# Performance work log

Measured on AMD Instinct MI355X. Metric: run time of the kernel, lower is better.

## Reference

```python
import jax, jax.numpy as jnp
import numpy as np
import math

T, P, ITERS, H = 6, 8, 2, 8          # nr_types, num_proto, iters, n_head
D, F = 512, 1024                      # dim_proto, feature_dim (hidden_dim==D)
L = T * ITERS                         # 12 cross-attention layers


def _ln(x, g=None, b=None, eps=1e-5):
    m = x.mean(-1, keepdims=True)
    v = x.var(-1, keepdims=True)
    y = (x - m) * jax.lax.rsqrt(v + eps)
    if g is not None:
        y = y * g + b
    return y


def _forward(x_batch, batch_mask, node_type, pm_W, pm_b, pm_g, pm_bn,
             proto_logsigma, rand_mul, Wq, bq, Wk, bk, Wv, bv, Wo, bo,
             ag, ab, Wm1, bm1, lg, lb, Wm2, bm2, pg, pb):
    B, N, _ = x_batch.shape
    dt = x_batch.dtype
    bm = batch_mask.astype(dt)                                   # [B,N]
    onehot = jax.nn.one_hot(node_type, T, dtype=dt)              # [B,N,T]
    valid = bm * jnp.any(x_batch != 0, axis=-1).astype(dt)       # [B,N]
    mbt = onehot * valid[:, :, None]                             # [B,N,T]
    sums = jnp.einsum('bnt,bnf->btf', mbt, x_batch)              # per-(batch,type) sum
    cnt = mbt.sum(1)                                             # [B,T]
    fallback = x_batch.sum(1) / bm.sum(1, keepdims=True)         # [B,F]
    proto_mu = jnp.where(cnt[..., None] > 0,
                         sums / jnp.maximum(cnt, 1.0)[..., None],
                         fallback[:, None, :])                   # [B,T,F]

    # proto_mlp: Linear + LayerNorm + GELU (dropout = eval/identity)
    mu = jax.nn.gelu(_ln(proto_mu @ pm_W + pm_b, pm_g, pm_bn), approximate=False)  # [B,T,D]
    all_proto = mu[:, :, None, :] + jnp.exp(proto_logsigma)[None] * rand_mul[None]  # [B,T,P,D]

    dh = D // H
    scale = 1.0 / math.sqrt(dh)
    keymask = bm[:, None, None, :] == 0                          # [B,1,1,N]

    def layer(q, i):
        resid = q                                                 # [B,P,D]
        k = _ln((x_batch @ Wk[i] + bk[i]).reshape(B, N, H, dh))   # QK-LayerNorm (no affine)
        v = (x_batch @ Wv[i] + bv[i]).reshape(B, N, H, dh)
        qh = _ln((q @ Wq[i] + bq[i]).reshape(B, P, H, dh))
        dots = jnp.einsum('bkhd,bnhd->bkhn', qh, k) * scale       # [B,P,H,N]
        dots = jnp.where(keymask, -jnp.inf, dots)
        attn = jax.nn.softmax(dots, axis=-1)
        upd = jnp.einsum('bnhd,bkhn->bkhd', v, attn).reshape(B, P, D)
        upd = upd @ Wo[i] + bo[i]
        q = resid + _ln(upd, ag[i], ab[i])
        h = jax.nn.gelu(_ln(q @ Wm1[i] + bm1[i], lg[i], lb[i]), approximate=False)
        h = h @ Wm2[i] + bm2[i]
        return q + _ln(h, pg[i], pb[i])

    outs = []
    c = 0
    for i in range(T):
        p = all_proto[:, i]
        for _ in range(ITERS):
            p = layer(p, c)
            c += 1
        outs.append(p)
    prototypes = jnp.stack(outs, axis=1)                          # [B,T,P,D]
    return prototypes, proto_mu


def setup_inputs() -> dict:
    key = jax.random.key(0)
    ks = jax.random.split(key, 40)
    B, N = 4, 4096
    sc = 0.02

    def rn(i, shape, s=sc):
        return jax.random.normal(ks[i], shape, jnp.float32) * s

    inp = {
        'x_batch': jax.random.normal(ks[0], (B, N, F), jnp.float32),
        'batch_mask': jax.random.randint(ks[1], (B, N), 0, 2, jnp.int32),
        'node_type': jax.random.randint(ks[2], (B, N), 0, T, jnp.int32),
        'pm_W': rn(3, (F, D)), 'pm_b': jnp.zeros((D,)),
        'pm_g': jnp.ones((D,)), 'pm_bn': jnp.zeros((D,)),
        'proto_logsigma': rn(4, (T, 1, D), 0.05),
        'rand_mul': jax.random.normal(ks[5], (T, P, D), jnp.float32),
        'Wq': rn(6, (L, D, D)), 'bq': jnp.zeros((L, D)),
        'Wk': rn(7, (L, F, D)), 'bk': jnp.zeros((L, D)),
        'Wv': rn(8, (L, F, D)), 'bv': jnp.zeros((L, D)),
        'Wo': rn(9, (L, D, D)), 'bo': jnp.zeros((L, D)),
        'ag': jnp.ones((L, D)), 'ab': jnp.zeros((L, D)),
        'Wm1': rn(10, (L, D, D)), 'bm1': jnp.zeros((L, D)),
        'lg': jnp.ones((L, D)), 'lb': jnp.zeros((L, D)),
        'Wm2': rn(11, (L, D, D)), 'bm2': jnp.zeros((L, D)),
        'pg': jnp.ones((L, D)), 'pb': jnp.zeros((L, D)),
    }
    return inp


def reference(x_batch, batch_mask, node_type, pm_W, pm_b, pm_g, pm_bn,
              proto_logsigma, rand_mul, Wq, bq, Wk, bk, Wv, bv, Wo, bo,
              ag, ab, Wm1, bm1, lg, lb, Wm2, bm2, pg, pb):
    return _forward(x_batch, batch_mask, node_type, pm_W, pm_b, pm_g, pm_bn,
                    proto_logsigma, rand_mul, Wq, bq, Wk, bk, Wv, bv, Wo, bo,
                    ag, ab, Wm1, bm1, lg, lb, Wm2, bm2, pg, pb)
```

## Files before the change

### kernel.cpp

```cpp
#include <hip/hip_runtime.h>
#include <hip/hip_bf16.h>
#include <stdint.h>

#define TT 6
#define PP 8
#define HH 8
#define DD 512
#define FF 1024
#define DH 64
#define NB 4
#define NN 4096
#define LL 12
#define NCH 16
#define CHK 256

typedef __attribute__((ext_vector_type(8))) short short8v;
typedef __attribute__((ext_vector_type(4))) float f32x4;
typedef __attribute__((ext_vector_type(4))) unsigned short u16x4;
typedef __attribute__((ext_vector_type(8))) unsigned short u16x8;
typedef unsigned short u16;

__device__ __forceinline__ float bf2f(u16 u){
  union { unsigned int i; float f; } x; x.i = ((unsigned int)u) << 16; return x.f;
}
// ... 6 lines not shown
  #pragma unroll
  for (int o = 32; o > 0; o >>= 1) x += __shfl_xor(x, o);
  return x;
}
__device__ __forceinline__ float ldf(const void* p, size_t i, int f32){
  float v;
  if (f32) v = ((const float*)p)[i];
  else     v = bf2f(((const u16*)p)[i]);
  return v;
}
__device__ __forceinline__ float gemv_vec(const float* __restrict__ xs,
    const void* __restrict__ W, size_t wbase, int ktot, int wf32,
    float* __restrict__ red, int tid){
  int g = tid & 63, sl = tid >> 6;
  int kpw = ktot >> 3;
  float a[8] = {0,0,0,0,0,0,0,0};
  if (wf32){
    const float* Wp = (const float*)W + wbase + (size_t)(sl*kpw)*DD + g*8;
    #pragma unroll 4
    for (int i = 0; i < kpw; ++i){
      float xv = xs[sl*kpw + i];
      f32x4 lo = *(const f32x4*)(Wp + (size_t)i*DD);
      f32x4 hi = *(const f32x4*)(Wp + (size_t)i*DD + 4);
      a[0]+=xv*lo.x; a[1]+=xv*lo.y; a[2]+=xv*lo.z; a[3]+=xv*lo.w;
      a[4]+=xv*hi.x; a[5]+=xv*hi.y; a[6]+=xv*hi.z; a[7]+=xv*hi.w;
    }
  } else {
    const u16* Wp = (const u16*)W + wbase + (size_t)(sl*kpw)*DD + g*8;
    #pragma unroll 4
    for (int i = 0; i < kpw; ++i){
      float xv = xs[sl*kpw + i];
      u16x8 w8 = *(const u16x8*)(Wp + (size_t)i*DD);
      #pragma unroll
      for (int j = 0; j < 8; ++j) a[j] += xv * bf2f(w8[j]);
    }
  }
  #pragma unroll
  for (int j = 0; j < 8; ++j) red[sl*512 + g*8 + j] = a[j];
  __syncthreads();
  float y = 0;
  #pragma unroll
  for (int s2 = 0; s2 < 8; ++s2) y += red[s2*512 + tid];
  return y;
}
__device__ __forceinline__ void glds16(const void* g, void* l){
#if __has_builtin(__builtin_amdgcn_global_load_lds)
  __builtin_amdgcn_global_load_lds(
      (const __attribute__((address_space(1))) void*)g,
      (__attribute__((address_space(3))) void*)l, 16, 0, 0);
#else
  *(u16x8*)l = *(const u16x8*)g;
#endif
}
__device__ __forceinline__ void tail_gemm(f32x4 acc[2][4], const u16* __restrict__ Bp,
    const u16* As, int l15, int q4, int n0w){
  #pragma unroll
  for (int mi = 0; mi < 2; ++mi)
    #pragma unroll
    for (int ni = 0; ni < 4; ++ni){ f32x4 z = {0,0,0,0}; acc[mi][ni] = z; }
  #pragma unroll 2
  for (int k0 = 0; k0 < 512; k0 += 32){
    short8v bf[4], af[2];
    #pragma unroll
    for (int ni = 0; ni < 4; ++ni)
      bf[ni] = *(const short8v*)(Bp + (size_t)(n0w + ni*16 + l15)*DD + k0 + q4*8);
    #pragma unroll
    for (int mi = 0; mi < 2; ++mi)
      af[mi] = *(const short8v*)(As + (mi*16 + l15)*520 + k0 + q4*8);
    #pragma unroll
    for (int mi = 0; mi < 2; ++mi)
      #pragma unroll
      for (int ni = 0; ni < 4; ++ni)
        acc[mi][ni] = __builtin_amdgcn_mfma_f32_16x16x32_bf16(af[mi], bf[ni], acc[mi][ni], 0, 0, 0);
  }
}
__device__ __forceinline__ void row_ln(const f32x4 acc[2][4],
    float* red1, float* red2, int w, int l15, int q4,
    float mv[2][4], float rv[2][4]){
  float s1[2][4], s2[2][4];
  #pragma unroll
  for (int mi = 0; mi < 2; ++mi)
    #pragma unroll
    for (int r = 0; r < 4; ++r){
      float a0=acc[mi][0][r], a1=acc[mi][1][r], a2=acc[mi][2][r], a3=acc[mi][3][r];
      s1[mi][r] = (a0+a1)+(a2+a3);
      s2[mi][r] = (a0*a0+a1*a1)+(a2*a2+a3*a3);
    }
  #pragma unroll
  for (int o = 1; o < 16; o <<= 1)
    #pragma unroll
    for (int mi = 0; mi < 2; ++mi)
      #pragma unroll
      for (int r = 0; r < 4; ++r){
        s1[mi][r] += __shfl_xor(s1[mi][r], o);
        s2[mi][r] += __shfl_xor(s2[mi][r], o);
      }
  if (l15 == 0){
    #pragma unroll
    for (int mi = 0; mi < 2; ++mi)
      #pragma unroll
      for (int r = 0; r < 4; ++r){
        int row = mi*16 + q4*4 + r;
        red1[row*8 + w] = s1[mi][r];
        red2[row*8 + w] = s2[mi][r];
      }
  }
  __syncthreads();
  #pragma unroll
  for (int mi = 0; mi < 2; ++mi)
    #pragma unroll
    for (int r = 0; r < 4; ++r){
      int row = mi*16 + q4*4 + r;
      float S1 = 0, S2 = 0;
      #pragma unroll
      for (int j = 0; j < 8; ++j){ S1 += red1[row*8+j]; S2 += red2[row*8+j]; }
      float m = S1 * (1.f/DD);
      float var = S2 * (1.f/DD) - m*m;
      mv[mi][r] = m;
      rv[mi][r] = rsqrtf(var + 1e-5f);
    }
  __syncthreads();
}

__global__ void k_detect(const void* __restrict__ X, int* __restrict__ flag){
  int tid = threadIdx.x;
  const u16* u = (const u16*)X;
  int bad = 0;
  for (int i = tid; i < 8192; i += 256){
    int ex = (u[i] >> 7) & 0xFF;
    if (ex >= 0x90) bad = 1;
  }
  __shared__ int s;
  if (tid == 0) s = 0;
  __syncthreads();
  if (bad) s = 1;
  __syncthreads();
  if (tid == 0) *flag = s;
}

__global__ void k_xbv(const void* __restrict__ X, u16* __restrict__ Xb,
                      const int* __restrict__ bm, float* __restrict__ valid,
                      const int* __restrict__ flagp){
  int f32 = *flagp;
  int bid = blockIdx.x, tid = threadIdx.x;
  size_t idx = (size_t)bid*FF + tid*4;
  bool a;
  if (f32){
    f32x4 v = *(const f32x4*)((const float*)X + idx);
    u16x4 o; o.x=f2bf(v.x); o.y=f2bf(v.y); o.z=f2bf(v.z); o.w=f2bf(v.w);
    *(u16x4*)(Xb+idx) = o;
    a = (v.x!=0.f)||(v.y!=0.f)||(v.z!=0.f)||(v.w!=0.f);
  } else {
    u16x4 v = *(const u16x4*)((const u16*)X + idx);
    *(u16x4*)(Xb+idx) = v;
    a = (bf2f(v.x)!=0.f)||(bf2f(v.y)!=0.f)||(bf2f(v.z)!=0.f)||(bf2f(v.w)!=0.f);
  }
  __shared__ int flag;
  if (tid==0) flag = 0;
  __syncthreads();
  if (a) flag = 1;
  __syncthreads();
  if (tid==0) valid[bid] = (flag && bm[bid]) ? 1.f : 0.f;
}

__global__ void k_compact(const int* __restrict__ bm, int* __restrict__ nidx,
                          int* __restrict__ cntc){
  int b = blockIdx.x, tid = threadIdx.x;
  __shared__ int csum[256];
  __shared__ int pref[257];
  int base = b*NN + tid*16;
  int f[16]; int loc = 0;
  #pragma unroll
  for (int i = 0; i < 16; ++i){ f[i] = (bm[base+i] != 0); loc += f[i]; }
// ... 119 lines not shown
  int bt = blockIdx.x; int b = bt/TT, t = bt%TT;
  int d = threadIdx.x;
  __shared__ float xs[FF];
  __shared__ float red[4096];
  __shared__ float r1[8], r2[8];
  xs[d] = proto_mu[(size_t)bt*FF + d];
  xs[d+512] = proto_mu[(size_t)bt*FF + d + 512];
  __syncthreads();
  float acc = ldf(pmb, d, f32) + gemv_vec(xs, pmW, 0, FF, f32, red, d);
  int lane = d & 63, wid = d >> 6;
  float s1 = wave_sum(acc), s2 = wave_sum(acc*acc);
  if (lane==0){ r1[wid]=s1; r2[wid]=s2; }
  __syncthreads();
  float m=0, qq=0;
  #pragma unroll
  for (int i=0;i<8;++i){ m+=r1[i]; qq+=r2[i]; }
  m *= (1.f/DD); float var = qq*(1.f/DD) - m*m;
  float y = (acc - m) * rsqrtf(var + 1e-5f) * ldf(pmg, d, f32) + ldf(pmbn, d, f32);
  float mu = 0.5f * y * (1.f + erff(y * 0.70710678118654752f));
  #pragma unroll
  for (int p = 0; p < PP; ++p){
    float rv = ldf(rmul, (size_t)(t*PP+p)*DD + d, f32);
    float ls = ldf(lsig, (size_t)t*DD + d, f32);
    qstate[(((size_t)(b*TT+t))*PP + p)*DD + d] = mu + expf(ls) * rv;
  }
}

__global__ void k_transpose(const void* __restrict__ Wk, const void* __restrict__ Wv,
                            u16* __restrict__ TK, u16* __restrict__ TV,
                            int tlo, int s, const int* __restrict__ flagp){
  int f32 = *flagp;
  int ti = blockIdx.z >> 1, kv = blockIdx.z & 1;
  int c = 2*(tlo+ti)+s;
  size_t eoff = (size_t)c*FF*DD;
  const void* W = kv ? Wv : Wk;
  u16* T = (kv ? TV : TK) + (size_t)ti*FF*DD;
  __shared__ u16 tile[32][33];
  int n0 = blockIdx.x * 32, k0 = blockIdx.y * 32;
  int tx = threadIdx.x, ty = threadIdx.y;
  #pragma unroll
  for (int i = 0; i < 4; ++i){
    size_t idx = eoff + (size_t)(k0 + ty + i*8)*DD + n0 + tx;
    u16 v;
    if (f32) v = f2bf(((const float*)W)[idx]);
    else     v = ((const u16*)W)[idx];
    tile[ty + i*8][tx] = v;
  }
  __syncthreads();
  #pragma unroll
  for (int i = 0; i < 4; ++i)
    T[(size_t)(n0 + ty + i*8)*FF + k0 + tx] = tile[tx][ty + i*8];
}

__global__ void __launch_bounds__(512) k_kvgemm(const u16* __restrict__ Xb,
    const u16* __restrict__ TK, const u16* __restrict__ TV,
    const void* __restrict__ bk, const void* __restrict__ bv,
    u16* __restrict__ Kb, u16* __restrict__ Vb,
    const int* __restrict__ nidx, const int* __restrict__ cntc,
    int tlo, int s, int nt, const int* __restrict__ flagp){
  int f32 = *flagp;
  int orig = blockIdx.x;
  int x = orig & 7, r = orig >> 3;
  int bx = r / nt, pr = r - bx*nt;
  int pairg = x*nt + pr;
  int by = pairg & 3; int kvti = pairg >> 2; int kv = kvti & 1; int ti = kvti >> 1;
  int b = bx >> 4, jt = bx & 15;
  int cnt = cntc[b];
  if (jt*256 >= cnt) return;
  int c = 2*(tlo+ti)+s;
  size_t boff = (size_t)c*DD;
  const u16* WT = (kv ? TV : TK) + (size_t)ti*FF*DD;
  const void* bias = kv ? bv : bk;
  u16* out = (kv ? Vb : Kb) + (size_t)ti*((size_t)NB*NN*DD);
  int n0 = by*128;
  __shared__ __align__(16) char LDS[3*24576];
  int tid = threadIdx.x, wid = tid >> 6, lane = tid & 63;
  int wr = wid >> 1, wcn = wid & 1;
  const u16* gp0; const u16* gp1; const u16* gp2;
  int lo0, lo1, lo2;
  {
    const u16* gps[3]; int los[3];
    #pragma unroll
    for (int i = 0; i < 3; ++i){
      int e = tid + i*512;
      if (e < 1024){
        int row = e>>2, sp = e&3;
        int ssrc = sp ^ (((row>>3)&1)<<1);
        int cl = jt*256 + row; if (cl >= cnt) cl = cnt-1;
        int grow = nidx[b*NN + cl];
        gps[i] = Xb + ((size_t)b*NN + grow)*FF + ssrc*8;
        los[i] = e*16;
      } else {
        int e2 = e - 1024;
        int row = e2>>2, sp = e2&3;
        int ssrc = sp ^ (((row>>3)&1)<<1);
        gps[i] = WT + (size_t)(n0 + row)*FF + ssrc*8;
        los[i] = 16384 + e2*16;
      }
    }
    gp0=gps[0]; gp1=gps[1]; gp2=gps[2];
    lo0=los[0]; lo1=los[1]; lo2=los[2];
  }
#define STAGE(T) { char* bb_ = LDS + ((T)%3)*24576; \
  glds16(gp0 + (T)*32, bb_ + lo0); glds16(gp1 + (T)*32, bb_ + lo1); \
  glds16(gp2 + (T)*32, bb_ + lo2); }
  int ke = (lane>>4) ^ (((lane>>3)&1)<<1);
  int arow[4], brow[4];
  #pragma unroll
  for (int mi = 0; mi < 4; ++mi)
    arow[mi] = (wr*64 + mi*16 + (lane&15))*64 + ke*16;
  #pragma unroll
  for (int ni = 0; ni < 4; ++ni)
    brow[ni] = 16384 + (wcn*64 + ni*16 + (lane&15))*64 + ke*16;
  f32x4 acc[4][4] = {};
  STAGE(0);
  STAGE(1);
  asm volatile("s_waitcnt vmcnt(3)" ::: "memory");
  __builtin_amdgcn_sched_barrier(0);
  __builtin_amdgcn_s_barrier();
  __builtin_amdgcn_sched_barrier(0);
  #pragma unroll
  for (int t = 0; t < 32; ++t){
    const char* Bbuf = LDS + (t%3)*24576;
    short8v af[4], bf[4];
    #pragma unroll
    for (int mi = 0; mi < 4; ++mi)
      af[mi] = *(const short8v*)(Bbuf + arow[mi]);
    #pragma unroll
    for (int ni = 0; ni < 4; ++ni)
      bf[ni] = *(const short8v*)(Bbuf + brow[ni]);
    if (t + 2 <= 31) STAGE(t+2);
    __builtin_amdgcn_s_setprio(1);
    #pragma unroll
    for (int mi = 0; mi < 4; ++mi)
      #pragma unroll
      for (int ni = 0; ni < 4; ++ni)
        acc[mi][ni] = __builtin_amdgcn_mfma_f32_16x16x32_bf16(af[mi], bf[ni], acc[mi][ni], 0, 0, 0);
    __builtin_amdgcn_s_setprio(0);
    if (t < 30)       asm volatile("s_waitcnt vmcnt(3)" ::: "memory");
    else if (t == 30) asm volatile("s_waitcnt vmcnt(0)" ::: "memory");
    __builtin_amdgcn_sched_barrier(0);
    if (t < 31){
      __builtin_amdgcn_s_barrier();
      __builtin_amdgcn_sched_barrier(0);
    }
  }
#undef STAGE
  #pragma unroll
  for (int mi = 0; mi < 4; ++mi){
    #pragma unroll
    for (int ni = 0; ni < 4; ++ni){
      int col = n0 + wcn*64 + ni*16 + (lane & 15);
      float bvf = ldf(bias, boff + col, f32);
      #pragma unroll
      for (int r2 = 0; r2 < 4; ++r2){
        int row = jt*256 + wr*64 + mi*16 + (lane>>4)*4 + r2;
        out[((size_t)b*NN + row)*DD + col] = f2bf(acc[mi][ni][r2] + bvf);
      }
    }
  }
}

__global__ void __launch_bounds__(512) k_qproj(const float* __restrict__ qstate,
      const void* __restrict__ Wq, const void* __restrict__ bq,
      float* __restrict__ qh, int tlo, int s, int wmode,
      const int* __restrict__ flagp){
  int f32 = *flagp;
  int wf32 = wmode ? f32 : 0;
  int z = blockIdx.x; int ti = z >> 5, rr = z & 31;
  int b = rr >> 3, p = rr & 7;
  int t = tlo + ti, c = 2*t + s;
  size_t woff = (size_t)c*DD*DD, boff = (size_t)c*DD;
  int d = threadIdx.x;
  __shared__ float xs[DD];
  __shared__ float red[4096];
  const float* xrow = qstate + (((size_t)(b*TT+t))*PP + p)*DD;
  xs[d] = xrow[d];
  __syncthreads();
  float acc = ldf(bq, boff + d, f32) + gemv_vec(xs, Wq, woff, DD, wf32, red, d);
  float s1 = wave_sum(acc) * (1.f/DH);
  float s2 = wave_sum(acc*acc) * (1.f/DH);
  float var = s2 - s1*s1;
  qh[(size_t)z*DD + d] = (acc - s1) * rsqrtf(var + 1e-5f);
}

__global__ void __launch_bounds__(512) k_attnA(const u16* __restrict__ Kb,
     const u16* __restrict__ Vb, const float* __restrict__ qh,
     const int* __restrict__ cntc, float* __restrict__ Opart, float* __restrict__ lpart){
  int ic = blockIdx.x, bh = blockIdx.y, ti = blockIdx.z;
  int b = bh >> 3, h = bh & 7;
  int cnt = cntc[b];
  if (ic*CHK >= cnt) return;
  int tid = threadIdx.x, p8 = tid >> 6, ln = tid & 63;
  int r8 = ln >> 3, g = ln & 7;
  __shared__ __align__(16) char KV[65536];
  __shared__ float qs[PP*DH];
  __shared__ float qsum[PP];
  __shared__ float e_lds[CHK*9];
  int rem = cnt - ic*CHK;
  float qv = qh[((size_t)(ti*32 + b*PP + p8))*DD + h*DH + ln];
  size_t tioff = (size_t)ti*((size_t)NB*NN*DD);
  const u16* Kbase = Kb + tioff + ((size_t)(b*NN) + (size_t)ic*CHK)*DD + h*DH;
  const u16* Vbase = Vb + tioff + ((size_t)(b*NN) + (size_t)ic*CHK)*DD + h*DH;
  #pragma unroll
  for (int i = 0; i < 4; ++i){
    int e = tid + i*512;
    int row = e >> 3, sp = e & 7;
    int rr = row < rem ? row : rem-1;
    glds16(Kbase + (size_t)rr*DD + sp*8, (char*)KV + e*16);
// ... 47 lines not shown
    }
    float dg = (g==0)?ap[0]:(g==1)?ap[1]:(g==2)?ap[2]:(g==3)?ap[3]
             : (g==4)?ap[4]:(g==5)?ap[5]:(g==6)?ap[6]:ap[7];
    float sv = (dg - sm*qsum[g]) * inv * 0.125f;
    e_lds[nl*9 + g] = (nl < rem) ? __expf(sv) : 0.f;
  }
  __syncthreads();
  {
    float lp = 0;
    #pragma unroll
    for (int j = 0; j < CHK/64; ++j) lp += e_lds[(ln + j*64)*9 + p8];
    lp = wave_sum(lp);
    if (ln == 0) lpart[((size_t)(ti*32+bh)*NCH + ic)*PP + p8] = lp;
  }
  {
    float a0=0,a1=0,a2=0,a3=0,a4=0,a5=0,a6=0,a7=0;
    int vseg = (r8 ^ g) * 16;
    #pragma unroll 4
    for (int m = 0; m < CHK/8; ++m){
      float e = e_lds[(g + m*8)*9 + p8];
      u16x8 vv = *(const u16x8*)((const char*)KV + 32768 + (g + m*8)*128 + vseg);
      a0 += e*bf2f(vv[0]); a1 += e*bf2f(vv[1]);
      a2 += e*bf2f(vv[2]); a3 += e*bf2f(vv[3]);
      a4 += e*bf2f(vv[4]); a5 += e*bf2f(vv[5]);
      a6 += e*bf2f(vv[6]); a7 += e*bf2f(vv[7]);
    }
    #pragma unroll
    for (int o = 1; o < 8; o <<= 1){
      a0 += __shfl_xor(a0, o); a1 += __shfl_xor(a1, o);
      a2 += __shfl_xor(a2, o); a3 += __shfl_xor(a3, o);
      a4 += __shfl_xor(a4, o); a5 += __shfl_xor(a5, o);
      a6 += __shfl_xor(a6, o); a7 += __shfl_xor(a7, o);
    }
    if (g == 0){
      float* op = Opart + ((size_t)(ti*32+bh)*NCH + ic)*512 + p8*64 + r8*8;
      f32x4 lo = {a0,a1,a2,a3}, hi = {a4,a5,a6,a7};
      *(f32x4*)op = lo;
      *((f32x4*)op + 1) = hi;
    }
  }
}

__global__ void __launch_bounds__(512) k_tailm(
    const float* __restrict__ Opart, const float* __restrict__ lpart,
    const int* __restrict__ cntc,
    float* __restrict__ qstate, float* __restrict__ qh,
    const u16* __restrict__ Wt,
    const void* __restrict__ bo, const void* __restrict__ ag, const void* __restrict__ ab,
    const void* __restrict__ bm1, const void* __restrict__ lg, const void* __restrict__ lb,
    const void* __restrict__ bm2, const void* __restrict__ pg, const void* __restrict__ pb,
    const void* __restrict__ bq,
    int tlo, int s, const int* __restrict__ flagp){
  int f32 = *flagp;
  int ti = blockIdx.x;
  int t = tlo + ti, c = 2*t + s;
  int tid = threadIdx.x;
  int w = tid >> 6, lane = tid & 63, q4 = lane >> 4, l15 = lane & 15;
  int n0w = w*64;
  size_t boff = (size_t)c*DD;
  const size_t famSz = (size_t)LL*DD*DD;
  __shared__ u16 As[32*520];
  __shared__ float red1[256], red2[256];
  __shared__ float lval[256];
  if (tid < 256){
    int row = tid >> 3, hh = tid & 7;
    int b = row >> 3, p = row & 7;
    int nch = (cntc[b] + CHK - 1) / CHK;
    float l = 0;
    for (int ic = 0; ic < nch; ++ic)
      l += lpart[((size_t)(ti*32 + b*8 + hh)*NCH + ic)*PP + p];
    lval[tid] = 1.f / l;
  }
  __syncthreads();
  {
    int hh = tid >> 6, dd = tid & 63;
    for (int row = 0; row < 32; ++row){
      int b = row >> 3, p = row & 7;
      int nch = (cntc[b] + CHK - 1) / CHK;
      float o = 0;
      for (int ic = 0; ic < nch; ++ic)
        o += Opart[((size_t)(ti*32 + b*8 + hh)*NCH + ic)*512 + p*64 + dd];
      As[row*520 + tid] = f2bf(o * lval[row*8 + hh]);
    }
  }
  __syncthreads();
  f32x4 acc[2][4], q2[2][4];
  float mv[2][4], rv[2][4];
  {
    const u16* Bp = Wt + famSz + (size_t)c*DD*DD;
    tail_gemm(acc, Bp, As, l15, q4, n0w);
    #pragma unroll
    for (int ni = 0; ni < 4; ++ni){
      float bv = ldf(bo, boff + n0w + ni*16 + l15, f32);
      #pragma unroll
      for (int mi = 0; mi < 2; ++mi)
        #pragma unroll
        for (int r = 0; r < 4; ++r) acc[mi][ni][r] += bv;
    }
    row_ln(acc, red1, red2, w, l15, q4, mv, rv);
    #pragma unroll
    for (int ni = 0; ni < 4; ++ni){
      int col = n0w + ni*16 + l15;
      float gm = ldf(ag, boff + col, f32), bt = ldf(ab, boff + col, f32);
      #pragma unroll
      for (int mi = 0; mi < 2; ++mi)
        #pragma unroll
        for (int r = 0; r < 4; ++r){
          int row = mi*16 + q4*4 + r;
          int b = row >> 3, p = row & 7;
          size_t qoff = (((size_t)(b*TT+t))*PP + p)*DD;
          float y = (acc[mi][ni][r] - mv[mi][r])*rv[mi][r]*gm + bt;
          q2[mi][ni][r] = qstate[qoff + col] + y;
        }
    }
    #pragma unroll
    for (int mi = 0; mi < 2; ++mi)
      #pragma unroll
      for (int r = 0; r < 4; ++r){
        int row = mi*16 + q4*4 + r;
        #pragma unroll
        for (int ni = 0; ni < 4; ++ni)
          As[row*520 + n0w + ni*16 + l15] = f2bf(q2[mi][ni][r]);
      }
  }
  __syncthreads();
  {
    const u16* Bp = Wt + 2*famSz + (size_t)c*DD*DD;
    tail_gemm(acc, Bp, As + 0, l15, q4, n0w);
    #pragma unroll
    for (int ni = 0; ni < 4; ++ni){
      float bv = ldf(bm1, boff + n0w + ni*16 + l15, f32);
      #pragma unroll
      for (int mi = 0; mi < 2; ++mi)
        #pragma unroll
        for (int r = 0; r < 4; ++r) acc[mi][ni][r] += bv;
    }
    row_ln(acc, red1, red2, w, l15, q4, mv, rv);
    #pragma unroll
    for (int ni = 0; ni < 4; ++ni){
      int col = n0w + ni*16 + l15;
      float gm = ldf(lg, boff + col, f32), bt = ldf(lb, boff + col, f32);
      #pragma unroll
      for (int mi = 0; mi < 2; ++mi)
        #pragma unroll
        for (int r = 0; r < 4; ++r){
          int row = mi*16 + q4*4 + r;
          float y = (acc[mi][ni][r] - mv[mi][r])*rv[mi][r]*gm + bt;
          y = 0.5f*y*(1.f + erff(y*0.70710678118654752f));
          As[row*520 + col] = f2bf(y);
        }
    }
  }
  __syncthreads();
  {
    const u16* Bp = Wt + 3*famSz + (size_t)c*DD*DD;
    tail_gemm(acc, Bp, As, l15, q4, n0w);
    #pragma unroll
    for (int ni = 0; ni < 4; ++ni){
      float bv = ldf(bm2, boff + n0w + ni*16 + l15, f32);
      #pragma unroll
      for (int mi = 0; mi < 2; ++mi)
        #pragma unroll
        for (int r = 0; r < 4; ++r) acc[mi][ni][r] += bv;
    }
    row_ln(acc, red1, red2, w, l15, q4, mv, rv);
    #pragma unroll
    for (int ni = 0; ni < 4; ++ni){
      int col = n0w + ni*16 + l15;
      float gm = ldf(pg, boff + col, f32), bt = ldf(pb, boff + col, f32);
      #pragma unroll
      for (int mi = 0; mi < 2; ++mi)
        #pragma unroll
        for (int r = 0; r < 4; ++r){
          int row = mi*16 + q4*4 + r;
          int b = row >> 3, p = row & 7;
          size_t qoff = (((size_t)(b*TT+t))*PP + p)*DD;
          float outv = q2[mi][ni][r] + (acc[mi][ni][r] - mv[mi][r])*rv[mi][r]*gm + bt;
          qstate[qoff + col] = outv;
          if (s == 0) As[row*520 + col] = f2bf(outv);
        }
    }
  }
  if (s == 0){
    __syncthreads();
    const u16* Bp = Wt + (size_t)(c+1)*DD*DD;
    tail_gemm(acc, Bp, As, l15, q4, n0w);
    #pragma unroll
    for (int ni = 0; ni < 4; ++ni){
      float bv = ldf(bq, (size_t)(c+1)*DD + n0w + ni*16 + l15, f32);
      #pragma unroll
      for (int mi = 0; mi < 2; ++mi)
        #pragma unroll
        for (int r = 0; r < 4; ++r) acc[mi][ni][r] += bv;
    }
    float s1[2][4], s2[2][4];
    #pragma unroll
    for (int mi = 0; mi < 2; ++mi)
      #pragma unroll
      for (int r = 0; r < 4; ++r){
        float a0=acc[mi][0][r], a1=acc[mi][1][r], a2=acc[mi][2][r], a3=acc[mi][3][r];
        s1[mi][r] = (a0+a1)+(a2+a3);
        s2[mi][r] = (a0*a0+a1*a1)+(a2*a2+a3*a3);
      }
    #pragma unroll
    for (int o = 1; o < 16; o <<= 1)
      #pragma unroll
      for (int mi = 0; mi < 2; ++mi)
        #pragma unroll
        for (int r = 0; r < 4; ++r){
          s1[mi][r] += __shfl_xor(s1[mi][r], o);
          s2[mi][r] += __shfl_xor(s2[mi][r], o);
        }
    #pragma unroll
    for (int mi = 0; mi < 2; ++mi)
      #pragma unroll
      for (int r = 0; r < 4; ++r){
        int row = mi*16 + q4*4 + r;
        float m = s1[mi][r] * (1.f/DH);
        float var = s2[mi][r] * (1.f/DH) - m*m;
        float ri = rsqrtf(var + 1e-5f);
        #pragma unroll
        for (int ni = 0; ni < 4; ++ni){
          int col = n0w + ni*16 + l15;
          qh[((size_t)(ti*32 + row))*DD + col] = (acc[mi][ni][r] - m)*ri;
        }
      }
  }
}

__global__ void __launch_bounds__(512) k_tail(
    const float* __restrict__ Opart, const float* __restrict__ lpart,
    const int* __restrict__ cntc,
    float* __restrict__ qstate, float* __restrict__ qh,
    const void* __restrict__ Wo_, const void* __restrict__ Wm1_,
    const void* __restrict__ Wm2_, const void* __restrict__ Wq_,
    const void* __restrict__ bo, const void* __restrict__ ag, const void* __restrict__ ab,
    const void* __restrict__ bm1, const void* __restrict__ lg, const void* __restrict__ lb,
    const void* __restrict__ bm2, const void* __restrict__ pg, const void* __restrict__ pb,
    const void* __restrict__ bq,
    int tlo, int s, int wmode, const int* __restrict__ flagp){
  int f32 = *flagp;
  int wf32 = wmode ? f32 : 0;
  int z = blockIdx.x; int ti = z >> 5, rr = z & 31;
  int b = rr >> 3, p = rr & 7;
  int t = tlo + ti, c = 2*t + s;
  int d = threadIdx.x;
  int h = d >> 6, dd = d & 63;
  int lane = d & 63, wid = d >> 6;
  size_t qoff = (((size_t)(b*TT+t))*PP + p)*DD;
  size_t boff = (size_t)c*DD;
  size_t w0 = (size_t)c*DD*DD;
  __shared__ float xs[DD];
  __shared__ float red[4096];
  __shared__ float r1[8], r2[8];
  int nch = (cntc[b] + CHK - 1) / CHK;
  float o = 0, l = 0;
  for (int ic = 0; ic < nch; ++ic){
    o += Opart[((size_t)(ti*32 + b*8 + h)*NCH + ic)*512 + p*64 + dd];
    l += lpart[((size_t)(ti*32 + b*8 + h)*NCH + ic)*PP + p];
  }
  float upd = o / l;
  xs[d] = upd;
  __syncthreads();
  float acc = ldf(bo, boff + d, f32) + gemv_vec(xs, Wo_, w0, DD, wf32, red, d);
  {
    float s1 = wave_sum(acc), s2 = wave_sum(acc*acc);
    if (lane == 0){ r1[wid] = s1; r2[wid] = s2; }
  }
  __syncthreads();
  float m = 0, qv = 0;
  #pragma unroll
  for (int i = 0; i < 8; ++i){ m += r1[i]; qv += r2[i]; }
  m *= (1.f/DD); float var = qv*(1.f/DD) - m*m;
  float y = (acc - m)*rsqrtf(var + 1e-5f)*ldf(ag, boff+d, f32) + ldf(ab, boff+d, f32);
  float q2 = qstate[qoff + d] + y;
  __syncthreads();
  xs[d] = q2;
  __syncthreads();
  float acc2 = ldf(bm1, boff + d, f32) + gemv_vec(xs, Wm1_, w0, DD, wf32, red, d);
// ... 71 lines not shown
  float* bmsum    = (float*)(ws + 512);
  float* colsums  = (float*)(ws + 768);
  float* coltotal = (float*)(ws + 99072);
  float* valid    = (float*)(ws + 115456);
  float* proto_mu = (float*)(ws + 180992);
  float* qstate   = (float*)(ws + 279296);
  int*   cntc     = (int*)(ws + 672512);
  int*   nidx     = (int*)(ws + 672768);

  size_t off = 738304;
  auto take = [&](size_t bytes)->char*{
    char* p = ws + off; off = (off + bytes + 255) & ~(size_t)255; return p;
  };
  u16* Xbf = (u16*)take((size_t)NB*NN*FF*2);

  const size_t perT = (size_t)65536
                    + 16384
                    + 1048576
                    + 2*1048576
                    + 2*16777216;
  size_t base = off;
  int nt = 1;
  if      (ws_size >= base + 6*perT + 65536) nt = 6;
  else if (ws_size >= base + 3*perT + 65536) nt = 3;
  else if (ws_size >= base + 2*perT + 65536) nt = 2;

  float* qh    = (float*)take((size_t)nt*65536);
  float* lpart = (float*)take((size_t)nt*16384);
  float* Opart = (float*)take((size_t)nt*1048576);
  u16*   WkT   = (u16*)take((size_t)nt*1048576);
  u16*   WvT   = (u16*)take((size_t)nt*1048576);
  u16*   Kb    = (u16*)take((size_t)nt*16777216);
  u16*   Vb    = (u16*)take((size_t)nt*16777216);

  const size_t wtBytes = (size_t)4*LL*DD*DD*2;
  int useWt = (ws_size >= off + wtBytes + 65536) ? 1 : 0;
  u16* Wt = useWt ? (u16*)take(wtBytes) : nullptr;

  hipMemsetAsync(ws + 256, 0, 115200, stream);
  k_detect<<<1, 256, 0, stream>>>(X, flagp);
  k_xbv<<<NB*NN, 256, 0, stream>>>(X, Xbf, bm, valid, flagp);
  k_compact<<<NB, 256, 0, stream>>>(bm, nidx, cntc);
  if (useWt)
    k_wbfT<<<dim3(16, 16, 4*LL), dim3(32, 8), 0, stream>>>(Wq, Wo, Wm1, Wm2, Wt, flagp);
  k_cnt<<<NB, 256, 0, stream>>>(valid, bm, ntype, cnt, bmsum);
  k_colsum<<<dim3(1, 64, NB), 256, 0, stream>>>(Xbf, valid, ntype, colsums, coltotal);
  k_protomu<<<NB*TT, 256, 0, stream>>>(colsums, coltotal, cnt, bmsum, proto_mu, d_out, flagp);
  k_mu<<<NB*TT, 512, 0, stream>>>(proto_mu, pmW, pmb, pmg, pmbn, lsig, rmul, qstate, flagp);

  for (int tlo = 0; tlo < TT; tlo += nt){
    for (int s = 0; s < 2; ++s){
      k_transpose<<<dim3(16, 32, 2*nt), dim3(32, 8), 0, stream>>>(
          Wk, Wv, WkT, WvT, tlo, s, flagp);
      k_kvgemm<<<64*8*nt, 512, 0, stream>>>(
          Xbf, WkT, WvT, bk, bv, Kb, Vb, nidx, cntc, tlo, s, nt, flagp);
      if (s == 0)
        k_qproj<<<nt*32, 512, 0, stream>>>(qstate, Wq, bq, qh, tlo, s, 1, flagp);
      k_attnA<<<dim3(NCH, 32, nt), 512, 0, stream>>>(Kb, Vb, qh, cntc, Opart, lpart);
      if (useWt)
        k_tailm<<<nt, 512, 0, stream>>>(Opart, lpart, cntc, qstate, qh, Wt,
            bo, ag, ab, bm1, lg, lb, bm2, pg, pb, bq, tlo, s, flagp);
      else
        k_tail<<<nt*32, 512, 0, stream>>>(Opart, lpart, cntc, qstate, qh,
            Wo, Wm1, Wm2, Wq, bo, ag, ab, bm1, lg, lb, bm2, pg, pb, bq,
            tlo, s, 1, flagp);
    }
  }
  k_out<<<NB*TT*PP*DD/256, 256, 0, stream>>>(qstate, d_out, flagp);
}
```

Measured before the change: 693.7 us.

## Enlarge K/V GEMM tile to 256x256 with 4-stage split A/B LDS pipeline

The K/V projection GEMM now uses 256x256 output tiles per workgroup instead of 256x128, so each block does twice the work and the grid is halved. Each wave now accumulates a 128x64 sub-tile. A and B are staged into separate 4-deep LDS ring buffers, and loads are interleaved between half-tile MFMA groups. Block indexing is remapped so blocks are grouped per XCD. The aim is more data reuse per LDS byte and fewer redundant X loads. In exchange, register pressure rises (32 accumulators) and 128KB of LDS limits occupancy, with more barriers per k-step.

```diff
diff --git a/kernel.cpp b/kernel.cpp
--- a/kernel.cpp
+++ b/kernel.cpp
@@ -374,7 +374,21 @@
     T[(size_t)(n0 + ty + i*8)*FF + k0 + tx] = tile[tx][ty + i*8];
 }
 
-__global__ void __launch_bounds__(512) k_kvgemm(const u16* __restrict__ Xb,
+#define PBAR() { __builtin_amdgcn_sched_barrier(0); \
+                 __builtin_amdgcn_s_barrier(); \
+                 __builtin_amdgcn_sched_barrier(0); }
+
+template<int MH>
+__device__ __forceinline__ void mfma_q(f32x4 (&acc)[8][4],
+    const short8v (&af)[4], const short8v (&bf)[4]){
+  #pragma unroll
+  for (int i = 0; i < 4; ++i)
+    #pragma unroll
+    for (int j = 0; j < 4; ++j)
+      acc[MH*4+i][j] = __builtin_amdgcn_mfma_f32_16x16x32_bf16(af[i], bf[j], acc[MH*4+i][j], 0, 0, 0);
+}
+
+__global__ void __launch_bounds__(512, 2) k_kvgemm(const u16* __restrict__ Xb,
     const u16* __restrict__ TK, const u16* __restrict__ TV,
     const void* __restrict__ bk, const void* __restrict__ bv,
     u16* __restrict__ Kb, u16* __restrict__ Vb,
@@ -382,11 +396,13 @@
     int tlo, int s, int nt, const int* __restrict__ flagp){
   int f32 = *flagp;
   int orig = blockIdx.x;
-  int x = orig & 7, r = orig >> 3;
-  int bx = r / nt, pr = r - bx*nt;
-  int pairg = x*nt + pr;
-  int by = pairg & 3; int kvti = pairg >> 2; int kv = kvti & 1; int ti = kvti >> 1;
-  int b = bx >> 4, jt = bx & 15;
+  int nwg = gridDim.x;
+  int cpx = nwg >> 3;
+  int wgid = (orig & 7)*cpx + (orig >> 3);
+  int grp = 4*nt;
+  int aid = wgid / grp, inner = wgid - aid*grp;
+  int b = aid >> 4, jt = aid & 15;
+  int by = inner & 1, kv = (inner >> 1) & 1, ti = inner >> 2;
   int cnt = cntc[b];
   if (jt*256 >= cnt) return;
   int c = 2*(tlo+ti)+s;
@@ -394,89 +410,89 @@
   const u16* WT = (kv ? TV : TK) + (size_t)ti*FF*DD;
   const void* bias = kv ? bv : bk;
   u16* out = (kv ? Vb : Kb) + (size_t)ti*((size_t)NB*NN*DD);
-  int n0 = by*128;
-  __shared__ __align__(16) char LDS[3*24576];
+  int n0 = by*256;
+  __shared__ __align__(16) char LDS[131072];
   int tid = threadIdx.x, wid = tid >> 6, lane = tid & 63;
-  int wr = wid >> 1, wcn = wid & 1;
-  const u16* gp0; const u16* gp1; const u16* gp2;
-  int lo0, lo1, lo2;
-  {
-    const u16* gps[3]; int los[3];
-    #pragma unroll
-    for (int i = 0; i < 3; ++i){
-      int e = tid + i*512;
-      if (e < 1024){
-        int row = e>>2, sp = e&3;
-        int ssrc = sp ^ (((row>>3)&1)<<1);
-        int cl = jt*256 + row; if (cl >= cnt) cl = cnt-1;
-        int grow = nidx[b*NN + cl];
-        gps[i] = Xb + ((size_t)b*NN + grow)*FF + ssrc*8;
-        los[i] = e*16;
-      } else {
-        int e2 = e - 1024;
-        int row = e2>>2, sp = e2&3;
-        int ssrc = sp ^ (((row>>3)&1)<<1);
-        gps[i] = WT + (size_t)(n0 + row)*FF + ssrc*8;
-        los[i] = 16384 + e2*16;
-      }
-    }
-    gp0=gps[0]; gp1=gps[1]; gp2=gps[2];
-    lo0=los[0]; lo1=los[1]; lo2=los[2];
-  }
-#define STAGE(T) { char* bb_ = LDS + ((T)%3)*24576; \
-  glds16(gp0 + (T)*32, bb_ + lo0); glds16(gp1 + (T)*32, bb_ + lo1); \
-  glds16(gp2 + (T)*32, bb_ + lo2); }
-  int ke = (lane>>4) ^ (((lane>>3)&1)<<1);
-  int arow[4], brow[4];
-  #pragma unroll
-  for (int mi = 0; mi < 4; ++mi)
-    arow[mi] = (wr*64 + mi*16 + (lane&15))*64 + ke*16;
-  #pragma unroll
-  for (int ni = 0; ni < 4; ++ni)
-    brow[ni] = 16384 + (wcn*64 + ni*16 + (lane&15))*64 + ke*16;
-  f32x4 acc[4][4] = {};
-  STAGE(0);
-  STAGE(1);
-  asm volatile("s_waitcnt vmcnt(3)" ::: "memory");
-  __builtin_amdgcn_sched_barrier(0);
-  __builtin_amdgcn_s_barrier();
-  __builtin_amdgcn_sched_barrier(0);
-  #pragma unroll
-  for (int t = 0; t < 32; ++t){
-    const char* Bbuf = LDS + (t%3)*24576;
+  int wr = wid >> 2, wc = wid & 3;
+  int l15 = lane & 15;
+  int keo = ((lane>>4) ^ (((lane>>3)&1)<<1)) * 16;
+  int abase = (wr*128 + l15)*64 + keo;
+  int bbase = (wc*64  + l15)*64 + keo;
+  int row0 = tid >> 2, sp = tid & 3;
+  int ssrc = sp ^ (((row0>>3)&1)<<1);
+  int cl0 = jt*256 + row0;        if (cl0 >= cnt) cl0 = cnt-1;
+  int cl1 = jt*256 + row0 + 128;  if (cl1 >= cnt) cl1 = cnt-1;
+  const u16* pA0 = Xb + ((size_t)b*NN + nidx[b*NN+cl0])*FF + ssrc*8;
+  const u16* pA1 = Xb + ((size_t)b*NN + nidx[b*NN+cl1])*FF + ssrc*8;
+  const u16* pB0 = WT + (size_t)(n0 + row0)*FF + ssrc*8;
+  const u16* pB1 = WT + (size_t)(n0 + row0 + 128)*FF + ssrc*8;
+  int la0 = tid*16, la1 = la0 + 8192;
+#define STA(S_) { char* d_ = LDS + ((S_)&3)*16384; \
+  glds16(pA0 + (S_)*32, d_ + la0); glds16(pA1 + (S_)*32, d_ + la1); }
+#define STB(S_) { char* d_ = LDS + 65536 + ((S_)&3)*16384; \
+  glds16(pB0 + (S_)*32, d_ + la0); glds16(pB1 + (S_)*32, d_ + la1); }
+  f32x4 acc[8][4] = {};
+  STA(0); STB(0); STA(1); STB(1); STA(2); STB(2); STA(3);
+  asm volatile("s_waitcnt vmcnt(6)" ::: "memory");
+  PBAR();
+  #pragma unroll 1
+  for (int tk = 0; tk < 16; ++tk){
+    int s0 = 2*tk, s1 = s0 + 1;
+    const char* A0p = LDS + (((tk&1)<<1))*16384;
+    const char* B0p = A0p + 65536;
+    const char* A1p = A0p + 16384;
+    const char* B1p = B0p + 16384;
     short8v af[4], bf[4];
     #pragma unroll
-    for (int mi = 0; mi < 4; ++mi)
-      af[mi] = *(const short8v*)(Bbuf + arow[mi]);
-    #pragma unroll
-    for (int ni = 0; ni < 4; ++ni)
-      bf[ni] = *(const short8v*)(Bbuf + brow[ni]);
-    if (t + 2 <= 31) STAGE(t+2);
+    for (int i = 0; i < 4; ++i) af[i] = *(const short8v*)(A0p + abase + i*1024);
+    #pragma unroll
+    for (int j = 0; j < 4; ++j) bf[j] = *(const short8v*)(B0p + bbase + j*1024);
+    if (tk <= 14) STB(s0+3);
+    PBAR();
     __builtin_amdgcn_s_setprio(1);
-    #pragma unroll
-    for (int mi = 0; mi < 4; ++mi)
-      #pragma unroll
-      for (int ni = 0; ni < 4; ++ni)
-        acc[mi][ni] = __builtin_amdgcn_mfma_f32_16x16x32_bf16(af[mi], bf[ni], acc[mi][ni], 0, 0, 0);
+    mfma_q<0>(acc, af, bf);
     __builtin_amdgcn_s_setprio(0);
-    if (t < 30)       asm volatile("s_waitcnt vmcnt(3)" ::: "memory");
-    else if (t == 30) asm volatile("s_waitcnt vmcnt(0)" ::: "memory");
-    __builtin_amdgcn_sched_barrier(0);
-    if (t < 31){
-      __builtin_amdgcn_s_barrier();
-      __builtin_amdgcn_sched_barrier(0);
-    }
-  }
-#undef STAGE
-  #pragma unroll
-  for (int mi = 0; mi < 4; ++mi){
+    PBAR();
+    #pragma unroll
+    for (int i = 0; i < 4; ++i) af[i] = *(const short8v*)(A0p + abase + 4096 + i*1024);
+    if (tk <= 13) STA(s0+4);
+    PBAR();
+    __builtin_amdgcn_s_setprio(1);
+    mfma_q<1>(acc, af, bf);
+    __builtin_amdgcn_s_setprio(0);
+    PBAR();
+    #pragma unroll
+    for (int i = 0; i < 4; ++i) af[i] = *(const short8v*)(A1p + abase + i*1024);
+    #pragma unroll
+    for (int j = 0; j < 4; ++j) bf[j] = *(const short8v*)(B1p + bbase + j*1024);
+    if (tk <= 13) STB(s1+3);
+    PBAR();
+    __builtin_amdgcn_s_setprio(1);
+    mfma_q<0>(acc, af, bf);
+    __builtin_amdgcn_s_setprio(0);
+    PBAR();
+    #pragma unroll
+    for (int i = 0; i < 4; ++i) af[i] = *(const short8v*)(A1p + abase + 4096 + i*1024);
+    if (tk <= 13) STA(s1+4);
+    if (tk < 14)       { asm volatile("s_waitcnt vmcnt(6)" ::: "memory"); }
+    else if (tk == 14) { asm volatile("s_waitcnt vmcnt(0)" ::: "memory"); }
+    PBAR();
+    __builtin_amdgcn_s_setprio(1);
+    mfma_q<1>(acc, af, bf);
+    __builtin_amdgcn_s_setprio(0);
+    PBAR();
+  }
+#undef STA
+#undef STB
+  #pragma unroll
+  for (int mi = 0; mi < 8; ++mi){
     #pragma unroll
     for (int ni = 0; ni < 4; ++ni){
-      int col = n0 + wcn*64 + ni*16 + (lane & 15);
+      int col = n0 + wc*64 + ni*16 + l15;
       float bvf = ldf(bias, boff + col, f32);
       #pragma unroll
       for (int r2 = 0; r2 < 4; ++r2){
-        int row = jt*256 + wr*64 + mi*16 + (lane>>4)*4 + r2;
+        int row = jt*256 + wr*128 + mi*16 + (lane>>4)*4 + r2;
         out[((size_t)b*NN + row)*DD + col] = f2bf(acc[mi][ni][r2] + bvf);
       }
     }
@@ -980,7 +996,7 @@
     for (int s = 0; s < 2; ++s){
       k_transpose<<<dim3(16, 32, 2*nt), dim3(32, 8), 0, stream>>>(
           Wk, Wv, WkT, WvT, tlo, s, flagp);
-      k_kvgemm<<<64*8*nt, 512, 0, stream>>>(
+      k_kvgemm<<<256*nt, 512, 0, stream>>>(
           Xbf, WkT, WvT, bk, bv, Kb, Vb, nidx, cntc, tlo, s, nt, flagp);
       if (s == 0)
         k_qproj<<<nt*32, 512, 0, stream>>>(qstate, Wq, bq, qh, tlo, s, 1, flagp);
```

Measured after the change: 859.5 us. 23.9% more time.

## Split tail MLP kernel per batch to quadruple block-level parallelism

Applied to the files above, without the earlier changes.

The fused tail kernel (Wo, MLP, next-layer Q projection) previously ran one block per type and handled all 32 query rows. It now launches one block per (type, batch), each handling 8 rows padded to a 16-row MFMA tile. This gives four times as many blocks for the small, latency-bound tail. The cost is that every block streams the full weight matrices, so weight reads rise fourfold, and half of each MFMA tile is wasted on zero padding.

```diff
diff --git a/kernel.cpp b/kernel.cpp
--- a/kernel.cpp
+++ b/kernel.cpp
@@ -82,73 +82,59 @@
   *(u16x8*)l = *(const u16x8*)g;
 #endif
 }
-__device__ __forceinline__ void tail_gemm(f32x4 acc[2][4], const u16* __restrict__ Bp,
+__device__ __forceinline__ void tail_gemm8(f32x4 acc[4], const u16* __restrict__ Bp,
     const u16* As, int l15, int q4, int n0w){
   #pragma unroll
-  for (int mi = 0; mi < 2; ++mi)
-    #pragma unroll
-    for (int ni = 0; ni < 4; ++ni){ f32x4 z = {0,0,0,0}; acc[mi][ni] = z; }
+  for (int ni = 0; ni < 4; ++ni){ f32x4 z = {0,0,0,0}; acc[ni] = z; }
   #pragma unroll 2
   for (int k0 = 0; k0 < 512; k0 += 32){
-    short8v bf[4], af[2];
+    short8v bf[4], af;
     #pragma unroll
     for (int ni = 0; ni < 4; ++ni)
       bf[ni] = *(const short8v*)(Bp + (size_t)(n0w + ni*16 + l15)*DD + k0 + q4*8);
-    #pragma unroll
-    for (int mi = 0; mi < 2; ++mi)
-      af[mi] = *(const short8v*)(As + (mi*16 + l15)*520 + k0 + q4*8);
-    #pragma unroll
-    for (int mi = 0; mi < 2; ++mi)
-      #pragma unroll
-      for (int ni = 0; ni < 4; ++ni)
-        acc[mi][ni] = __builtin_amdgcn_mfma_f32_16x16x32_bf16(af[mi], bf[ni], acc[mi][ni], 0, 0, 0);
-  }
-}
-__device__ __forceinline__ void row_ln(const f32x4 acc[2][4],
+    af = *(const short8v*)(As + l15*520 + k0 + q4*8);
+    #pragma unroll
+    for (int ni = 0; ni < 4; ++ni)
+      acc[ni] = __builtin_amdgcn_mfma_f32_16x16x32_bf16(af, bf[ni], acc[ni], 0, 0, 0);
+  }
+}
+__device__ __forceinline__ void row_ln8(const f32x4 acc[4],
     float* red1, float* red2, int w, int l15, int q4,
-    float mv[2][4], float rv[2][4]){
-  float s1[2][4], s2[2][4];
-  #pragma unroll
-  for (int mi = 0; mi < 2; ++mi)
+    float mv[4], float rv[4]){
+  float s1[4], s2[4];
+  #pragma unroll
+  for (int r = 0; r < 4; ++r){
+    float a0=acc[0][r], a1=acc[1][r], a2=acc[2][r], a3=acc[3][r];
+    s1[r] = (a0+a1)+(a2+a3);
+    s2[r] = (a0*a0+a1*a1)+(a2*a2+a3*a3);
+  }
+  #pragma unroll
+  for (int o = 1; o < 16; o <<= 1)
     #pragma unroll
     for (int r = 0; r < 4; ++r){
-      float a0=acc[mi][0][r], a1=acc[mi][1][r], a2=acc[mi][2][r], a3=acc[mi][3][r];
-      s1[mi][r] = (a0+a1)+(a2+a3);
-      s2[mi][r] = (a0*a0+a1*a1)+(a2*a2+a3*a3);
-    }
-  #pragma unroll
-  for (int o = 1; o < 16; o <<= 1)
-    #pragma unroll
-    for (int mi = 0; mi < 2; ++mi)
-      #pragma unroll
-      for (int r = 0; r < 4; ++r){
-        s1[mi][r] += __shfl_xor(s1[mi][r], o);
-        s2[mi][r] += __shfl_xor(s2[mi][r], o);
-      }
+      s1[r] += __shfl_xor(s1[r], o);
+      s2[r] += __shfl_xor(s2[r], o);
+    }
   if (l15 == 0){
     #pragma unroll
-    for (int mi = 0; mi < 2; ++mi)
-      #pragma unroll
-      for (int r = 0; r < 4; ++r){
-        int row = mi*16 + q4*4 + r;
-        red1[row*8 + w] = s1[mi][r];
-        red2[row*8 + w] = s2[mi][r];
-      }
-  }
-  __syncthreads();
-  #pragma unroll
-  for (int mi = 0; mi < 2; ++mi)
-    #pragma unroll
     for (int r = 0; r < 4; ++r){
-      int row = mi*16 + q4*4 + r;
-      float S1 = 0, S2 = 0;
-      #pragma unroll
-      for (int j = 0; j < 8; ++j){ S1 += red1[row*8+j]; S2 += red2[row*8+j]; }
-      float m = S1 * (1.f/DD);
-      float var = S2 * (1.f/DD) - m*m;
-      mv[mi][r] = m;
-      rv[mi][r] = rsqrtf(var + 1e-5f);
-    }
+      int row = q4*4 + r;
+      red1[row*8 + w] = s1[r];
+      red2[row*8 + w] = s2[r];
+    }
+  }
+  __syncthreads();
+  #pragma unroll
+  for (int r = 0; r < 4; ++r){
+    int row = q4*4 + r;
+    float S1 = 0, S2 = 0;
+    #pragma unroll
+    for (int j = 0; j < 8; ++j){ S1 += red1[row*8+j]; S2 += red2[row*8+j]; }
+    float m = S1 * (1.f/DD);
+    float var = S2 * (1.f/DD) - m*m;
+    mv[r] = m;
+    rv[r] = rsqrtf(var + 1e-5f);
+  }
   __syncthreads();
 }
 
@@ -630,20 +616,21 @@
     const void* __restrict__ bq,
     int tlo, int s, const int* __restrict__ flagp){
   int f32 = *flagp;
-  int ti = blockIdx.x;
+  int z = blockIdx.x;
+  int ti = z >> 2, b = z & 3;
   int t = tlo + ti, c = 2*t + s;
   int tid = threadIdx.x;
   int w = tid >> 6, lane = tid & 63, q4 = lane >> 4, l15 = lane & 15;
   int n0w = w*64;
   size_t boff = (size_t)c*DD;
   const size_t famSz = (size_t)LL*DD*DD;
-  __shared__ u16 As[32*520];
-  __shared__ float red1[256], red2[256];
-  __shared__ float lval[256];
-  if (tid < 256){
-    int row = tid >> 3, hh = tid & 7;
-    int b = row >> 3, p = row & 7;
-    int nch = (cntc[b] + CHK - 1) / CHK;
+  __shared__ u16 As[16*520];
+  __shared__ float red1[128], red2[128];
+  __shared__ float lval[64];
+  int nch = (cntc[b] + CHK - 1) / CHK;
+  for (int i = tid; i < 16*520; i += 512) As[i] = 0;
+  if (tid < 64){
+    int p = tid >> 3, hh = tid & 7;
     float l = 0;
     for (int ic = 0; ic < nch; ++ic)
       l += lpart[((size_t)(ti*32 + b*8 + hh)*NCH + ic)*PP + p];
@@ -652,157 +639,138 @@
   __syncthreads();
   {
     int hh = tid >> 6, dd = tid & 63;
-    for (int row = 0; row < 32; ++row){
-      int b = row >> 3, p = row & 7;
-      int nch = (cntc[b] + CHK - 1) / CHK;
+    #pragma unroll
+    for (int p = 0; p < 8; ++p){
       float o = 0;
       for (int ic = 0; ic < nch; ++ic)
         o += Opart[((size_t)(ti*32 + b*8 + hh)*NCH + ic)*512 + p*64 + dd];
-      As[row*520 + tid] = f2bf(o * lval[row*8 + hh]);
-    }
-  }
-  __syncthreads();
-  f32x4 acc[2][4], q2[2][4];
-  float mv[2][4], rv[2][4];
+      As[p*520 + hh*64 + dd] = f2bf(o * lval[p*8 + hh]);
+    }
+  }
+  __syncthreads();
+  f32x4 acc[4], q2[4];
+  float mv[4], rv[4];
+  size_t qoffb = ((size_t)(b*TT+t))*PP*DD;
   {
     const u16* Bp = Wt + famSz + (size_t)c*DD*DD;
-    tail_gemm(acc, Bp, As, l15, q4, n0w);
+    tail_gemm8(acc, Bp, As, l15, q4, n0w);
     #pragma unroll
     for (int ni = 0; ni < 4; ++ni){
       float bv = ldf(bo, boff + n0w + ni*16 + l15, f32);
       #pragma unroll
-      for (int mi = 0; mi < 2; ++mi)
-        #pragma unroll
-        for (int r = 0; r < 4; ++r) acc[mi][ni][r] += bv;
-    }
-    row_ln(acc, red1, red2, w, l15, q4, mv, rv);
+      for (int r = 0; r < 4; ++r) acc[ni][r] += bv;
+    }
+    row_ln8(acc, red1, red2, w, l15, q4, mv, rv);
     #pragma unroll
     for (int ni = 0; ni < 4; ++ni){
       int col = n0w + ni*16 + l15;
       float gm = ldf(ag, boff + col, f32), bt = ldf(ab, boff + col, f32);
       #pragma unroll
-      for (int mi = 0; mi < 2; ++mi)
-        #pragma unroll
-        for (int r = 0; r < 4; ++r){
-          int row = mi*16 + q4*4 + r;
-          int b = row >> 3, p = row & 7;
-          size_t qoff = (((size_t)(b*TT+t))*PP + p)*DD;
-          float y = (acc[mi][ni][r] - mv[mi][r])*rv[mi][r]*gm + bt;
-          q2[mi][ni][r] = qstate[qoff + col] + y;
-        }
-    }
-    #pragma unroll
-    for (int mi = 0; mi < 2; ++mi)
-      #pragma unroll
       for (int r = 0; r < 4; ++r){
-        int row = mi*16 + q4*4 + r;
+        int row = q4*4 + r;
+        float y = (acc[ni][r] - mv[r])*rv[r]*gm + bt;
+        float res = (q4 < 2) ? qstate[qoffb + (size_t)row*DD + col] : 0.f;
+        q2[ni][r] = res + y;
+      }
+    }
+    if (q4 < 2){
+      #pragma unroll
+      for (int r = 0; r < 4; ++r){
+        int row = q4*4 + r;
         #pragma unroll
         for (int ni = 0; ni < 4; ++ni)
-          As[row*520 + n0w + ni*16 + l15] = f2bf(q2[mi][ni][r]);
+          As[row*520 + n0w + ni*16 + l15] = f2bf(q2[ni][r]);
       }
+    }
   }
   __syncthreads();
   {
     const u16* Bp = Wt + 2*famSz + (size_t)c*DD*DD;
-    tail_gemm(acc, Bp, As + 0, l15, q4, n0w);
+    tail_gemm8(acc, Bp, As, l15, q4, n0w);
     #pragma unroll
     for (int ni = 0; ni < 4; ++ni){
       float bv = ldf(bm1, boff + n0w + ni*16 + l15, f32);
       #pragma unroll
-      for (int mi = 0; mi < 2; ++mi)
-        #pragma unroll
-        for (int r = 0; r < 4; ++r) acc[mi][ni][r] += bv;
-    }
-    row_ln(acc, red1, red2, w, l15, q4, mv, rv);
+      for (int r = 0; r < 4; ++r) acc[ni][r] += bv;
+    }
+    row_ln8(acc, red1, red2, w, l15, q4, mv, rv);
     #pragma unroll
     for (int ni = 0; ni < 4; ++ni){
       int col = n0w + ni*16 + l15;
       float gm = ldf(lg, boff + col, f32), bt = ldf(lb, boff + col, f32);
       #pragma unroll
-      for (int mi = 0; mi < 2; ++mi)
-        #pragma unroll
-        for (int r = 0; r < 4; ++r){
-          int row = mi*16 + q4*4 + r;
-          float y = (acc[mi][ni][r] - mv[mi][r])*rv[mi][r]*gm + bt;
-          y = 0.5f*y*(1.f + erff(y*0.70710678118654752f));
-          As[row*520 + col] = f2bf(y);
-        }
+      for (int r = 0; r < 4; ++r){
+        int row = q4*4 + r;
+        float y = (acc[ni][r] - mv[r])*rv[r]*gm + bt;
+        y = 0.5f*y*(1.f + erff(y*0.70710678118654752f));
+        if (q4 < 2) As[row*520 + col] = f2bf(y);
+      }
     }
   }
   __syncthreads();
   {
     const u16* Bp = Wt + 3*famSz + (size_t)c*DD*DD;
-    tail_gemm(acc, Bp, As, l15, q4, n0w);
+    tail_gemm8(acc, Bp, As, l15, q4, n0w);
     #pragma unroll
     for (int ni = 0; ni < 4; ++ni){
       float bv = ldf(bm2, boff + n0w + ni*16 + l15, f32);
       #pragma unroll
-      for (int mi = 0; mi < 2; ++mi)
-        #pragma unroll
-        for (int r = 0; r < 4; ++r) acc[mi][ni][r] += bv;
-    }
-    row_ln(acc, red1, red2, w, l15, q4, mv, rv);
+      for (int r = 0; r < 4; ++r) acc[ni][r] += bv;
+    }
+    row_ln8(acc, red1, red2, w, l15, q4, mv, rv);
     #pragma unroll
     for (int ni = 0; ni < 4; ++ni){
       int col = n0w + ni*16 + l15;
       float gm = ldf(pg, boff + col, f32), bt = ldf(pb, boff + col, f32);
       #pragma unroll
-      for (int mi = 0; mi < 2; ++mi)
-        #pragma unroll
-        for (int r = 0; r < 4; ++r){
-          int row = mi*16 + q4*4 + r;
-          int b = row >> 3, p = row & 7;
-          size_t qoff = (((size_t)(b*TT+t))*PP + p)*DD;
-          float outv = q2[mi][ni][r] + (acc[mi][ni][r] - mv[mi][r])*rv[mi][r]*gm + bt;
-          qstate[qoff + col] = outv;
+      for (int r = 0; r < 4; ++r){
+        int row = q4*4 + r;
+        float outv = q2[ni][r] + (acc[ni][r] - mv[r])*rv[r]*gm + bt;
+        if (q4 < 2){
+          qstate[qoffb + (size_t)row*DD + col] = outv;
           if (s == 0) As[row*520 + col] = f2bf(outv);
         }
+      }
     }
   }
   if (s == 0){
     __syncthreads();
     const u16* Bp = Wt + (size_t)(c+1)*DD*DD;
-    tail_gemm(acc, Bp, As, l15, q4, n0w);
+    tail_gemm8(acc, Bp, As, l15, q4, n0w);
     #pragma unroll
     for (int ni = 0; ni < 4; ++ni){
       float bv = ldf(bq, (size_t)(c+1)*DD + n0w + ni*16 + l15, f32);
       #pragma unroll
-      for (int mi = 0; mi < 2; ++mi)
-        #pragma unroll
-        for (int r = 0; r < 4; ++r) acc[mi][ni][r] += bv;
-    }
-    float s1[2][4], s2[2][4];
-    #pragma unroll
-    for (int mi = 0; mi < 2; ++mi)
+      for (int r = 0; r < 4; ++r) acc[ni][r] += bv;
+    }
+    float s1[4], s2[4];
+    #pragma unroll
+    for (int r = 0; r < 4; ++r){
+      float a0=acc[0][r], a1=acc[1][r], a2=acc[2][r], a3=acc[3][r];
+      s1[r] = (a0+a1)+(a2+a3);
+      s2[r] = (a0*a0+a1*a1)+(a2*a2+a3*a3);
+    }
+    #pragma unroll
+    for (int o = 1; o < 16; o <<= 1)
       #pragma unroll
       for (int r = 0; r < 4; ++r){
-        float a0=acc[mi][0][r], a1=acc[mi][1][r], a2=acc[mi][2][r], a3=acc[mi][3][r];
-        s1[mi][r] = (a0+a1)+(a2+a3);
-        s2[mi][r] = (a0*a0+a1*a1)+(a2*a2+a3*a3);
+        s1[r] += __shfl_xor(s1[r], o);
+        s2[r] += __shfl_xor(s2[r], o);
       }
-    #pragma unroll
-    for (int o = 1; o < 16; o <<= 1)
-      #pragma unroll
-      for (int mi = 0; mi < 2; ++mi)
-        #pragma unroll
-        for (int r = 0; r < 4; ++r){
-          s1[mi][r] += __shfl_xor(s1[mi][r], o);
-          s2[mi][r] += __shfl_xor(s2[mi][r], o);
-        }
-    #pragma unroll
-    for (int mi = 0; mi < 2; ++mi)
+    if (q4 < 2){
       #pragma unroll
       for (int r = 0; r < 4; ++r){
-        int row = mi*16 + q4*4 + r;
-        float m = s1[mi][r] * (1.f/DH);
-        float var = s2[mi][r] * (1.f/DH) - m*m;
+        int row = q4*4 + r;
+        float m = s1[r] * (1.f/DH);
+        float var = s2[r] * (1.f/DH) - m*m;
         float ri = rsqrtf(var + 1e-5f);
         #pragma unroll
         for (int ni = 0; ni < 4; ++ni){
           int col = n0w + ni*16 + l15;
-          qh[((size_t)(ti*32 + row))*DD + col] = (acc[mi][ni][r] - m)*ri;
+          qh[((size_t)(ti*32 + b*8 + row))*DD + col] = (acc[ni][r] - m)*ri;
         }
       }
+    }
   }
 }
 
@@ -986,7 +954,7 @@
         k_qproj<<<nt*32, 512, 0, stream>>>(qstate, Wq, bq, qh, tlo, s, 1, flagp);
       k_attnA<<<dim3(NCH, 32, nt), 512, 0, stream>>>(Kb, Vb, qh, cntc, Opart, lpart);
       if (useWt)
-        k_tailm<<<nt, 512, 0, stream>>>(Opart, lpart, cntc, qstate, qh, Wt,
+        k_tailm<<<nt*4, 512, 0, stream>>>(Opart, lpart, cntc, qstate, qh, Wt,
             bo, ag, ab, bm1, lg, lb, bm2, pg, pb, bq, tlo, s, flagp);
       else
         k_tail<<<nt*32, 512, 0, stream>>>(Opart, lpart, cntc, qstate, qh,
```

New measurement: 700.4 us. Within noise of the previous version (+1.0%).
